# Performance work log

Measured on AMD Instinct MI355X. Metric: run time of the kernel, lower is better.

Reference implementation:

```python
import jax, jax.numpy as jnp
import numpy as np

EMBED_DIM = 1024
ATTN_DIM = 1024
BATCH = 4
SEQ = 2048


def setup_inputs() -> dict:
    key = jax.random.key(0)
    k1, k2, k3, k4 = jax.random.split(key, 4)
    embedded = jax.random.normal(k1, (BATCH, SEQ, EMBED_DIM), dtype=jnp.float32)
    # torch Linear weights have shape [out_features, in_features]
    scale = 1.0 / np.sqrt(EMBED_DIM)
    W_K = jax.random.uniform(k2, (ATTN_DIM, EMBED_DIM), dtype=jnp.float32, minval=-scale, maxval=scale)
    W_Q = jax.random.uniform(k3, (ATTN_DIM, EMBED_DIM), dtype=jnp.float32, minval=-scale, maxval=scale)
    W_V = jax.random.uniform(k4, (ATTN_DIM, EMBED_DIM), dtype=jnp.float32, minval=-scale, maxval=scale)
    return {"embedded": embedded, "W_K": W_K, "W_Q": W_Q, "W_V": W_V}


def reference(embedded, W_K, W_Q, W_V):
    # embedded: [B, L, E]; W_*: [A, E] (torch Linear layout, applied as x @ W.T)
    L = embedded.shape[1]
    A = W_K.shape[0]
    K = jnp.einsum('ble,ae->bla', embedded, W_K)
    Q = jnp.einsum('ble,ae->bla', embedded, W_Q)
    V = jnp.einsum('ble,ae->bla', embedded, W_V)
    att = jnp.einsum('bqa,bka->bqk', Q, K) / jnp.sqrt(jnp.float32(A))  # [B, L, L]
    causal = jnp.tril(jnp.ones((L, L), dtype=bool))  # lower-triangular mask
    att = jnp.where(causal, att, -jnp.inf)
    att = jax.nn.softmax(att, axis=-1)
    return jnp.einsum('bqk,bka->bqa', att, V)
```

## Files before the change

### kernel.cpp

```cpp
#include <hip/hip_runtime.h>
#include <hip/hip_bf16.h>
#include <stdint.h>

#define BATCH 4
#define SEQ   2048
#define EMB   1024
#define ADIM  1024

typedef __attribute__((ext_vector_type(8))) short  short8;
typedef __attribute__((ext_vector_type(4))) float  float4v;

static __device__ __forceinline__ unsigned short f2bf(float f) {
    unsigned int u = __float_as_uint(f);
    u += 0x7FFFu + ((u >> 16) & 1u);
    return (unsigned short)(u >> 16);
}

static __device__ __forceinline__ uint2 pack4(float4v v) {
    uint2 r;
    r.x = (unsigned)f2bf(v.x) | ((unsigned)f2bf(v.y) << 16);
    r.y = (unsigned)f2bf(v.z) | ((unsigned)f2bf(v.w) << 16);
    return r;
}

static __device__ __forceinline__ void gload16(const void* g, void* l) {
    __builtin_amdgcn_global_load_lds(
        (const __attribute__((address_space(1))) void*)g,
        (__attribute__((address_space(3))) void*)l, 16, 0, 0);
}

__global__ __launch_bounds__(256) void zero_kernel(float* __restrict__ p)
{
    const int i = (blockIdx.x * 256 + threadIdx.x) * 4;
    *(float4v*)(p + i) = float4v{0.f, 0.f, 0.f, 0.f};
}

__global__ __launch_bounds__(256) void cvt_all_kernel(
    const float* __restrict__ X,  const float* __restrict__ Wk,
    const float* __restrict__ Wq, const float* __restrict__ Wv,
    unsigned short* __restrict__ Xb,  unsigned short* __restrict__ Wkb,
    unsigned short* __restrict__ Wqb, unsigned short* __restrict__ Wvb)
{
    const int bI = blockIdx.x;
    const float* src; unsigned short* dst; int off;
    if (bI < 4096)      { src = X;  dst = Xb;  off = bI; }
    else if (bI < 4608) { src = Wk; dst = Wkb; off = bI - 4096; }
    else if (bI < 5120) { src = Wq; dst = Wqb; off = bI - 4608; }
    else                { src = Wv; dst = Wvb; off = bI - 5120; }
    const int i = (off * 256 + threadIdx.x) * 8;
    float4v a = *(const float4v*)(src + i);
    float4v b = *(const float4v*)(src + i + 4);
    uint2 pa = pack4(a), pb = pack4(b);
    uint4 o; o.x = pa.x; o.y = pa.y; o.z = pb.x; o.w = pb.y;
    *(uint4*)(dst + i) = o;
}

static __device__ __forceinline__ void gemm_core(
    const unsigned short* __restrict__ A, const unsigned short* __restrict__ B,
    int lda, int ldb, int m0, int n0, int kend,
    unsigned short* As, unsigned short* Bs, float4v acc[4][4])
{
    const int tid  = threadIdx.x;
    const int r    = tid >> 2;
    const int c8   = (tid & 3) << 3;
    const int lane = tid & 63;
    const int wave = tid >> 6;
    const int quad = lane >> 4;
    const int l16  = lane & 15;
    const int wm   = (wave >> 1) << 6;
    const int wn   = (wave & 1) << 6;

    const unsigned short* Ag = A + (size_t)(m0 + r) * lda + c8;
    const unsigned short* Bg = B + (size_t)(n0 + r) * ldb + c8;
    unsigned short* Al = As + tid * 8;
    unsigned short* Bl = Bs + tid * 8;

    for (int k0 = 0; k0 < kend; k0 += 64) {
        gload16(Ag + k0,                         Al);
        gload16(Ag + k0 + (size_t)64 * lda,      Al + 64 * 32);
        gload16(Ag + k0 + 32,                    Al + 4096);
        gload16(Ag + k0 + 32 + (size_t)64 * lda, Al + 4096 + 64 * 32);
        gload16(Bg + k0,                         Bl);
        gload16(Bg + k0 + (size_t)64 * ldb,      Bl + 64 * 32);
        gload16(Bg + k0 + 32,                    Bl + 4096);
        gload16(Bg + k0 + 32 + (size_t)64 * ldb, Bl + 4096 + 64 * 32);
        __syncthreads();

        #pragma unroll
        for (int h = 0; h < 2; ++h) {
            const unsigned short* Ah = As + h * 4096;
            const unsigned short* Bh = Bs + h * 4096;
            short8 af[4], bfr[4];
            #pragma unroll
            for (int i = 0; i < 4; ++i)
                af[i] = *(const short8*)&Ah[(wm + 16 * i + l16) * 32 + quad * 8];
            #pragma unroll
            for (int j = 0; j < 4; ++j)
                bfr[j] = *(const short8*)&Bh[(wn + 16 * j + l16) * 32 + quad * 8];
            #pragma unroll
            for (int i = 0; i < 4; ++i)
                #pragma unroll
                for (int j = 0; j < 4; ++j)
                    acc[i][j] = __builtin_amdgcn_mfma_f32_16x16x32_bf16(af[i], bfr[j], acc[i][j], 0, 0, 0);
        }
        __syncthreads();
    }
}

#define DECL_TILE_IDX() \
    const int lane = threadIdx.x & 63; \
    const int wave = threadIdx.x >> 6; \
    const int quad = lane >> 4; \
    const int l16  = lane & 15; \
    const int wm   = (wave >> 1) << 6; \
    const int wn   = (wave & 1) << 6;

__global__ __launch_bounds__(256) void qkv_kernel(
    const unsigned short* __restrict__ Xb, const unsigned short* __restrict__ Wqb,
    const unsigned short* __restrict__ Wkb, const unsigned short* __restrict__ Wvb,
    unsigned short* __restrict__ Qb, unsigned short* __restrict__ Kb,
    unsigned short* __restrict__ Vtb)
{
    __shared__ __align__(16) unsigned short As[2 * 128 * 32];
    __shared__ __align__(16) unsigned short Bs[2 * 128 * 32];
    const int m0 = blockIdx.y * 128;
    const int n0 = blockIdx.x * 128;
    const int z  = blockIdx.z;
    const unsigned short* W = (z == 0) ? Wqb : (z == 1) ? Wkb : Wvb;

    float4v acc[4][4];
    #pragma unroll
    for (int i = 0; i < 4; ++i)
        #pragma unroll
        for (int j = 0; j < 4; ++j)
            acc[i][j] = float4v{0.f, 0.f, 0.f, 0.f};

    gemm_core(Xb, W, EMB, EMB, m0, n0, EMB, As, Bs, acc);

    DECL_TILE_IDX();
    #pragma unroll
    for (int i = 0; i < 4; ++i)
        #pragma unroll
        for (int j = 0; j < 4; ++j)
            #pragma unroll
            for (int rr = 0; rr < 4; ++rr) {
                const int row = m0 + wm + 16 * i + quad * 4 + rr;
                const int col = n0 + wn + 16 * j + l16;
                const unsigned short v = f2bf(acc[i][j][rr]);
                if (z == 0)      Qb[(size_t)row * ADIM + col] = v;
                else if (z == 1) Kb[(size_t)row * ADIM + col] = v;
                else {
                    const int bb = row >> 11;
                    const int l  = row & (SEQ - 1);
                    Vtb[((size_t)(bb * ADIM + col) << 11) + l] = v;
                }
            }
}

__global__ __launch_bounds__(256) void s_kernel(
    const unsigned short* __restrict__ Qb, const unsigned short* __restrict__ Kb,
    unsigned short* __restrict__ E, float* __restrict__ rowsum)
{
    const int idx = blockIdx.x;
    const int b   = idx & 3;
    const int tri = idx >> 2;
    int qt = 0;
    while (((qt + 1) * (qt + 2)) / 2 <= tri) ++qt;
    const int kt = tri - (qt * (qt + 1)) / 2;
    const int q0 = qt << 7;
    const int k0 = kt << 7;

    __shared__ __align__(16) unsigned short As[2 * 128 * 32];
    __shared__ __align__(16) unsigned short Bs[2 * 128 * 32];

    float4v acc[4][4];
    #pragma unroll
    for (int i = 0; i < 4; ++i)
        #pragma unroll
        for (int j = 0; j < 4; ++j)
            acc[i][j] = float4v{0.f, 0.f, 0.f, 0.f};

    gemm_core(Qb + (size_t)b * SEQ * ADIM, Kb + (size_t)b * SEQ * ADIM,
              ADIM, ADIM, q0, k0, ADIM, As, Bs, acc);

    unsigned short* Eb = E + (size_t)b * SEQ * SEQ;
    float* rsb = rowsum + (size_t)b * SEQ;
    DECL_TILE_IDX();
    const float scale = 0.03125f;
    #pragma unroll
    for (int i = 0; i < 4; ++i)
        #pragma unroll
        for (int rr = 0; rr < 4; ++rr) {
            const int row = q0 + wm + 16 * i + quad * 4 + rr;
            float s = 0.f;
            #pragma unroll
            for (int j = 0; j < 4; ++j) {
                const int col = k0 + wn + 16 * j + l16;
                float e = (col <= row) ? __expf(acc[i][j][rr] * scale) : 0.f;
                s += e;
                Eb[(size_t)row * SEQ + col] = f2bf(e);
            }
            s += __shfl_xor(s, 1);
            s += __shfl_xor(s, 2);
            s += __shfl_xor(s, 4);
            s += __shfl_xor(s, 8);
            if (l16 == 0) atomicAdd(&rsb[row], s);
        }
}

__global__ __launch_bounds__(256) void pv_kernel(
    const unsigned short* __restrict__ E, const unsigned short* __restrict__ Vtb,
    const float* __restrict__ rowsum, float* __restrict__ out)
{
    const int idx = blockIdx.x;
    const int t   = 15 - (idx >> 5);
    const int rem = idx & 31;
    const int b   = rem >> 3;
    const int a0  = (rem & 7) << 7;
    const int q0  = t << 7;

    __shared__ __align__(16) unsigned short As[2 * 128 * 32];
    __shared__ __align__(16) unsigned short Bs[2 * 128 * 32];

    float4v acc[4][4];
    #pragma unroll
    for (int i = 0; i < 4; ++i)
        #pragma unroll
        for (int j = 0; j < 4; ++j)
            acc[i][j] = float4v{0.f, 0.f, 0.f, 0.f};

    gemm_core(E + (size_t)b * SEQ * SEQ, Vtb + (size_t)b * ADIM * SEQ,
              SEQ, SEQ, q0, a0, q0 + 128, As, Bs, acc);

    float* ob = out + (size_t)b * SEQ * ADIM;
    const float* rsb = rowsum + (size_t)b * SEQ;
    DECL_TILE_IDX();
    #pragma unroll
    for (int i = 0; i < 4; ++i)
        #pragma unroll
        for (int rr = 0; rr < 4; ++rr) {
            const int row = q0 + wm + 16 * i + quad * 4 + rr;
            const float inv = 1.0f / rsb[row];
            #pragma unroll
            for (int j = 0; j < 4; ++j) {
                const int col = a0 + wn + 16 * j + l16;
                ob[(size_t)row * ADIM + col] = acc[i][j][rr] * inv;
            }
        }
}

extern "C" void kernel_launch(void* const* d_in, const int* in_sizes, int n_in,
                              void* d_out, int out_size, void* d_ws, size_t ws_size,
                              hipStream_t stream)
{
    const float* X  = (const float*)d_in[0];
    const float* Wk = (const float*)d_in[1];
    const float* Wq = (const float*)d_in[2];
    const float* Wv = (const float*)d_in[3];
    float* out = (float*)d_out;

    const size_t MB = 1024 * 1024;
    char* ws = (char*)d_ws;
    unsigned short* Xb  = (unsigned short*)(ws);
    unsigned short* Wqb = (unsigned short*)(ws + 16 * MB);
    unsigned short* Wkb = (unsigned short*)(ws + 18 * MB);
    unsigned short* Wvb = (unsigned short*)(ws + 20 * MB);
    unsigned short* E   = (unsigned short*)(ws);
    unsigned short* Qb  = (unsigned short*)(ws + 64 * MB);
    unsigned short* Kb  = (unsigned short*)(ws + 80 * MB);
    unsigned short* Vtb = (unsigned short*)(ws + 96 * MB);
    float*          rowsum = (float*)(ws + 112 * MB);

    hipLaunchKernelGGL(zero_kernel, dim3(BATCH * SEQ / 1024), dim3(256), 0, stream, rowsum);
    hipLaunchKernelGGL(cvt_all_kernel, dim3(5632), dim3(256), 0, stream,
                       X, Wk, Wq, Wv, Xb, Wkb, Wqb, Wvb);
    hipLaunchKernelGGL(qkv_kernel, dim3(ADIM / 128, (BATCH * SEQ) / 128, 3), dim3(256), 0, stream,
                       Xb, Wqb, Wkb, Wvb, Qb, Kb, Vtb);
    hipLaunchKernelGGL(s_kernel, dim3(4 * 136), dim3(256), 0, stream, Qb, Kb, E, rowsum);
    hipLaunchKernelGGL(pv_kernel, dim3(512), dim3(256), 0, stream, E, Vtb, rowsum, out);
}
```

Before: 261.6 us.

## Triple-buffer GEMM core with async prefetch and swizzle QKV block order

Replaces the single-stage load/sync/compute loop in the shared GEMM core with a three-stage LDS ring. Global-to-LDS loads for iteration k+2 are issued before computing on iteration k, using explicit vmcnt waits and raw barriers. This is meant to hide global memory latency behind MFMA work. It also remaps the QKV grid to a 1D index with M-blocks grouped for L2 reuse, and sets launch_bounds occupancy hints. The trade-off is more LDS per block and reliance on hand-tuned waitcnt counts, which must match the gload16 implementation for correctness.

```diff
diff --git a/kernel.cpp b/kernel.cpp
--- a/kernel.cpp
+++ b/kernel.cpp
@@ -74,37 +74,49 @@
     const unsigned short* Bg = B + (size_t)(n0 + r) * ldb + c8;
     unsigned short* Al = As + tid * 8;
     unsigned short* Bl = Bs + tid * 8;
-
-    for (int k0 = 0; k0 < kend; k0 += 64) {
-        gload16(Ag + k0,                         Al);
-        gload16(Ag + k0 + (size_t)64 * lda,      Al + 64 * 32);
-        gload16(Ag + k0 + 32,                    Al + 4096);
-        gload16(Ag + k0 + 32 + (size_t)64 * lda, Al + 4096 + 64 * 32);
-        gload16(Bg + k0,                         Bl);
-        gload16(Bg + k0 + (size_t)64 * ldb,      Bl + 64 * 32);
-        gload16(Bg + k0 + 32,                    Bl + 4096);
-        gload16(Bg + k0 + 32 + (size_t)64 * ldb, Bl + 4096 + 64 * 32);
-        __syncthreads();
-
-        #pragma unroll
-        for (int h = 0; h < 2; ++h) {
-            const unsigned short* Ah = As + h * 4096;
-            const unsigned short* Bh = Bs + h * 4096;
-            short8 af[4], bfr[4];
-            #pragma unroll
-            for (int i = 0; i < 4; ++i)
-                af[i] = *(const short8*)&Ah[(wm + 16 * i + l16) * 32 + quad * 8];
+    const int niter = kend >> 5;
+
+    #define ISSUE(k0, st) do { \
+        unsigned short* al_ = Al + (st) * 4096; \
+        unsigned short* bl_ = Bl + (st) * 4096; \
+        gload16(Ag + (k0),                        al_); \
+        gload16(Ag + (k0) + (size_t)64 * lda,     al_ + 2048); \
+        gload16(Bg + (k0),                        bl_); \
+        gload16(Bg + (k0) + (size_t)64 * ldb,     bl_ + 2048); \
+    } while (0)
+
+    ISSUE(0, 0);
+    ISSUE(32, 1);
+
+    int ci = 0;
+    int ii = 2;
+    for (int it = 0; it < niter; ++it) {
+        const int knext = (it + 2 < niter) ? ((it + 2) << 5) : 0;
+        ISSUE(knext, ii);
+        asm volatile("s_waitcnt vmcnt(8)" ::: "memory");
+        asm volatile("s_barrier" ::: "memory");
+
+        const unsigned short* Ah = As + ci * 4096;
+        const unsigned short* Bh = Bs + ci * 4096;
+        short8 af[4], bfr[4];
+        #pragma unroll
+        for (int i = 0; i < 4; ++i)
+            af[i] = *(const short8*)&Ah[(wm + 16 * i + l16) * 32 + quad * 8];
+        #pragma unroll
+        for (int j = 0; j < 4; ++j)
+            bfr[j] = *(const short8*)&Bh[(wn + 16 * j + l16) * 32 + quad * 8];
+        #pragma unroll
+        for (int i = 0; i < 4; ++i)
             #pragma unroll
             for (int j = 0; j < 4; ++j)
-                bfr[j] = *(const short8*)&Bh[(wn + 16 * j + l16) * 32 + quad * 8];
-            #pragma unroll
-            for (int i = 0; i < 4; ++i)
-                #pragma unroll
-                for (int j = 0; j < 4; ++j)
-                    acc[i][j] = __builtin_amdgcn_mfma_f32_16x16x32_bf16(af[i], bfr[j], acc[i][j], 0, 0, 0);
-        }
-        __syncthreads();
+                acc[i][j] = __builtin_amdgcn_mfma_f32_16x16x32_bf16(af[i], bfr[j], acc[i][j], 0, 0, 0);
+
+        asm volatile("s_barrier" ::: "memory");
+        ci = (ci == 2) ? 0 : ci + 1;
+        ii = (ii == 2) ? 0 : ii + 1;
     }
+    asm volatile("s_waitcnt vmcnt(0)" ::: "memory");
+    #undef ISSUE
 }
 
 #define DECL_TILE_IDX() \
@@ -115,17 +127,21 @@
     const int wm   = (wave >> 1) << 6; \
     const int wn   = (wave & 1) << 6;
 
-__global__ __launch_bounds__(256) void qkv_kernel(
+__global__ __launch_bounds__(256, 3) void qkv_kernel(
     const unsigned short* __restrict__ Xb, const unsigned short* __restrict__ Wqb,
     const unsigned short* __restrict__ Wkb, const unsigned short* __restrict__ Wvb,
     unsigned short* __restrict__ Qb, unsigned short* __restrict__ Kb,
     unsigned short* __restrict__ Vtb)
 {
-    __shared__ __align__(16) unsigned short As[2 * 128 * 32];
-    __shared__ __align__(16) unsigned short Bs[2 * 128 * 32];
-    const int m0 = blockIdx.y * 128;
-    const int n0 = blockIdx.x * 128;
-    const int z  = blockIdx.z;
+    __shared__ __align__(16) unsigned short As[3 * 128 * 32];
+    __shared__ __align__(16) unsigned short Bs[3 * 128 * 32];
+    const int idx   = blockIdx.x;
+    const int mlow  = idx & 7;
+    const int n0    = ((idx >> 3) & 7) << 7;
+    const int rest  = idx >> 6;
+    const int mhigh = rest & 7;
+    const int z     = rest >> 3;
+    const int m0    = ((mhigh << 3) | mlow) << 7;
     const unsigned short* W = (z == 0) ? Wqb : (z == 1) ? Wkb : Wvb;
 
     float4v acc[4][4];
@@ -157,7 +173,7 @@
             }
 }
 
-__global__ __launch_bounds__(256) void s_kernel(
+__global__ __launch_bounds__(256, 3) void s_kernel(
     const unsigned short* __restrict__ Qb, const unsigned short* __restrict__ Kb,
     unsigned short* __restrict__ E, float* __restrict__ rowsum)
 {
@@ -170,8 +186,8 @@
     const int q0 = qt << 7;
     const int k0 = kt << 7;
 
-    __shared__ __align__(16) unsigned short As[2 * 128 * 32];
-    __shared__ __align__(16) unsigned short Bs[2 * 128 * 32];
+    __shared__ __align__(16) unsigned short As[3 * 128 * 32];
+    __shared__ __align__(16) unsigned short Bs[3 * 128 * 32];
 
     float4v acc[4][4];
     #pragma unroll
@@ -208,7 +224,7 @@
         }
 }
 
-__global__ __launch_bounds__(256) void pv_kernel(
+__global__ __launch_bounds__(256, 3) void pv_kernel(
     const unsigned short* __restrict__ E, const unsigned short* __restrict__ Vtb,
     const float* __restrict__ rowsum, float* __restrict__ out)
 {
@@ -219,8 +235,8 @@
     const int a0  = (rem & 7) << 7;
     const int q0  = t << 7;
 
-    __shared__ __align__(16) unsigned short As[2 * 128 * 32];
-    __shared__ __align__(16) unsigned short Bs[2 * 128 * 32];
+    __shared__ __align__(16) unsigned short As[3 * 128 * 32];
+    __shared__ __align__(16) unsigned short Bs[3 * 128 * 32];
 
     float4v acc[4][4];
     #pragma unroll
@@ -274,7 +290,7 @@
     hipLaunchKernelGGL(zero_kernel, dim3(BATCH * SEQ / 1024), dim3(256), 0, stream, rowsum);
     hipLaunchKernelGGL(cvt_all_kernel, dim3(5632), dim3(256), 0, stream,
                        X, Wk, Wq, Wv, Xb, Wkb, Wqb, Wvb);
-    hipLaunchKernelGGL(qkv_kernel, dim3(ADIM / 128, (BATCH * SEQ) / 128, 3), dim3(256), 0, stream,
+    hipLaunchKernelGGL(qkv_kernel, dim3(1536), dim3(256), 0, stream,
                        Xb, Wqb, Wkb, Wvb, Qb, Kb, Vtb);
     hipLaunchKernelGGL(s_kernel, dim3(4 * 136), dim3(256), 0, stream, Qb, Kb, E, rowsum);
     hipLaunchKernelGGL(pv_kernel, dim3(512), dim3(256), 0, stream, E, Vtb, rowsum, out);
```

Result: faster. 252.0 us (-3.7%).
